# Kernel optimization log

Measured on AMD Instinct MI355X. Metric: run time of the kernel, lower is better.

Reference implementation:

```python
import jax, jax.numpy as jnp
import numpy as np

B, T, D = 32, 512, 1024
N = 65536
H, L = 150, 17


def setup_inputs() -> dict:
    key = jax.random.key(0)
    ks = jax.random.split(key, 5)
    xs = jax.random.normal(ks[0], (B, T, D), dtype=jnp.float32)
    spans = jax.random.randint(ks[1], (N, 2), 0, T, dtype=jnp.int64 if jax.config.jax_enable_x64 else jnp.int32)
    batch_ids = jax.random.randint(ks[2], (N,), 0, B, dtype=spans.dtype)
    W1 = jax.random.normal(ks[3], (2 * D, H), dtype=jnp.float32) / np.sqrt(2 * D)
    b1 = jnp.zeros((H,), dtype=jnp.float32)
    W2 = jax.random.normal(ks[4], (H, L), dtype=jnp.float32) / np.sqrt(H)
    b2 = jnp.zeros((L,), dtype=jnp.float32)
    return {"xs": xs, "spans": spans, "batch_ids": batch_ids,
            "W1": W1, "b1": b1, "W2": W2, "b2": b2}


def reference(xs, spans, batch_ids, W1, b1, W2, b2):
    # Flatten batch/time: xs_flat [B*T, D]; offset span indices into flat space,
    # mirroring `idxs + max_length * i` in the torch forward.
    d = xs.shape[-1]
    xs_flat = xs.reshape(-1, d)
    flat_idx = spans + batch_ids[:, None] * xs.shape[1]  # [N, 2]
    # feature == 'concat': gather begin/end token reps and concat -> [N, 2D]
    feats = xs_flat[flat_idx.reshape(-1)].reshape(flat_idx.shape[0], 2 * d)
    h = jax.nn.relu(feats @ W1 + b1)  # MLP hidden layer (dropout p=0)
    scores = h @ W2 + b2              # output layer, no activation
    return scores  # [N, num_labels]; torch.split is a zero-copy view, omitted
```

## Files before the change

### kernel.cpp

```cpp
#include <hip/hip_runtime.h>
#include <stdint.h>

#define TT 512
#define DD 1024
#define NN 65536
#define HH 150
#define LL 17

typedef __bf16 bf16_t;
typedef short shortx8 __attribute__((ext_vector_type(8)));
typedef short shortx4 __attribute__((ext_vector_type(4)));
typedef float f32x4 __attribute__((ext_vector_type(4)));

typedef __attribute__((address_space(1))) const void gconst_void;
typedef __attribute__((address_space(3))) void lds_void;

static __device__ __forceinline__ short f2bf(float f) {
  return (short)__builtin_bit_cast(unsigned short, (bf16_t)f);
}

__global__ __launch_bounds__(256) void prep_all(
    const float* __restrict__ xs, const float* __restrict__ W1,
    const float* __restrict__ W2, short* __restrict__ xs16,
    short* __restrict__ Bp, short* __restrict__ W2p, int do_cvt)
{
  int b = blockIdx.x;
  if (do_cvt && b < 2048) {
    int t = b * 256 + threadIdx.x;
#pragma unroll
    for (int i = 0; i < 8; ++i) {
      int id = t + i * 524288;
      f32x4 v = reinterpret_cast<const f32x4*>(xs)[id];
      shortx4 o;
      o[0] = f2bf(v[0]); o[1] = f2bf(v[1]); o[2] = f2bf(v[2]); o[3] = f2bf(v[3]);
      reinterpret_cast<shortx4*>(xs16)[id] = o;
    }
    return;
  }
  int rb = do_cvt ? b - 2048 : b;
  int task = rb * 256 + threadIdx.x;
  const int NW1 = 64 * 10 * 64;
  if (task < NW1) {
    int kb  = task / 640;
    int rem = task - kb * 640;
    int cb = rem >> 6, l = rem & 63;
    int col  = cb * 16 + (l & 15);
    int krow = kb * 32 + (l >> 4) * 8;
    shortx8 v;
#pragma unroll
    for (int j = 0; j < 8; ++j) {
      float f = (col < HH) ? W1[(krow + j) * HH + col] : 0.f;
      v[j] = f2bf(f);
    }
    *reinterpret_cast<shortx8*>(Bp + task * 8) = v;
  } else if (task < NW1 + 640) {
    int t2 = task - NW1;
    int kb  = t2 >> 7;
    int rem = t2 & 127;
    int cb = rem >> 6, l = rem & 63;
    int col  = cb * 16 + (l & 15);
    int krow = kb * 32 + (l >> 4) * 8;
    shortx8 v;
#pragma unroll
    for (int j = 0; j < 8; ++j) {
      int r = krow + j;
      float f = (r < HH && col < LL) ? W2[r * LL + col] : 0.f;
      v[j] = f2bf(f);
    }
    *reinterpret_cast<shortx8*>(W2p + t2 * 8) = v;
  }
}

__device__ __forceinline__ void stageB(const short* __restrict__ Bp, char* lds,
                                       int c, int p, int wv, int lane) {
#pragma unroll
  for (int i = 0; i < 5; ++i) {
    const char* g = (const char*)Bp + (size_t)c * 20480 + wv * 5120 + i * 1024 + lane * 16;
    char* l = lds + p * 20480 + wv * 5120 + i * 1024;
    __builtin_amdgcn_global_load_lds((gconst_void*)g, (lds_void*)l, 16, 0, 0);
  }
}

template<int XS16>
__device__ __forceinline__ void loadA(const char* const (&abase)[2][2], int c,
                                      int kg, shortx8 (&abuf)[2][2]) {
  const int side = (c >= 16) ? 1 : 0;
#pragma unroll
  for (int rf = 0; rf < 2; ++rf) {
#pragma unroll
    for (int s = 0; s < 2; ++s) {
      int ks31 = (2 * c + s) & 31;
      if constexpr (XS16) {
        abuf[rf][s] = *reinterpret_cast<const shortx8*>(
            abase[rf][side] + ks31 * 64 + kg * 16);
      } else {
        f32x4 x = *reinterpret_cast<const f32x4*>(abase[rf][side] + ks31 * 128 + kg * 32);
        f32x4 y = *reinterpret_cast<const f32x4*>(abase[rf][side] + ks31 * 128 + kg * 32 + 16);
        shortx8 t;
        t[0]=f2bf(x[0]); t[1]=f2bf(x[1]); t[2]=f2bf(x[2]); t[3]=f2bf(x[3]);
        t[4]=f2bf(y[0]); t[5]=f2bf(y[1]); t[6]=f2bf(y[2]); t[7]=f2bf(y[3]);
        abuf[rf][s] = t;
      }
    }
  }
}

__device__ __forceinline__ void computeC(const char* lds, int p, int lane,
                                         const shortx8 (&abuf)[2][2],
                                         f32x4 (&acc)[2][10]) {
#pragma unroll
  for (int s = 0; s < 2; ++s) {
    shortx8 bfr[10];
#pragma unroll
    for (int cb = 0; cb < 10; ++cb)
      bfr[cb] = *reinterpret_cast<const shortx8*>(
          lds + p * 20480 + (s * 10 + cb) * 1024 + lane * 16);
#pragma unroll
    for (int rf = 0; rf < 2; ++rf)
#pragma unroll
      for (int cb = 0; cb < 10; ++cb)
        acc[rf][cb] = __builtin_amdgcn_mfma_f32_16x16x32_bf16(
            abuf[rf][s], bfr[cb], acc[rf][cb], 0, 0, 0);
  }
}

template<int XS16>
__global__ __launch_bounds__(256, 1) void span_mlp2(
    const void* __restrict__ xsv, const int* __restrict__ spans,
    const int* __restrict__ bids, const short* __restrict__ Bp,
    const float* __restrict__ b1, const short* __restrict__ W2p,
    const float* __restrict__ b2, float* __restrict__ out)
{
  __shared__ __align__(16) char lds[43008];

  const int tid  = threadIdx.x;
  const int wv   = tid >> 6;
  const int lane = tid & 63;
  const int l15  = lane & 15;
  const int kg   = lane >> 4;
  const int blk  = blockIdx.x;

  const char* abase[2][2];
  const int elt = XS16 ? 2 : 4;
#pragma unroll
  for (int rf = 0; rf < 2; ++rf) {
    int r  = blk * 128 + wv * 32 + rf * 16 + l15;
    int bb = bids[r];
    int s0 = spans[2 * r + 0];
    int s1 = spans[2 * r + 1];
    abase[rf][0] = (const char*)xsv + (size_t)(bb * TT + s0) * DD * elt;
    abase[rf][1] = (const char*)xsv + (size_t)(bb * TT + s1) * DD * elt;
  }

  f32x4 acc[2][10];
  {
    f32x4 z = {0.f, 0.f, 0.f, 0.f};
#pragma unroll
    for (int rf = 0; rf < 2; ++rf)
#pragma unroll
      for (int cb = 0; cb < 10; ++cb) acc[rf][cb] = z;
  }

  shortx8 abufA[2][2], abufB[2][2];

#define WAITSTAGE() do { \
    if constexpr (XS16) asm volatile("s_waitcnt vmcnt(4)" ::: "memory"); \
    else                asm volatile("s_waitcnt vmcnt(8)" ::: "memory"); \
    __builtin_amdgcn_s_barrier(); \
    __builtin_amdgcn_sched_barrier(0); \
  } while (0)

  stageB(Bp, lds, 0, 0, wv, lane);
  loadA<XS16>(abase, 0, kg, abufA);
  WAITSTAGE();

  for (int cp = 0; cp < 16; ++cp) {
    int c0 = 2 * cp;
    stageB(Bp, lds, c0 + 1, 1, wv, lane);
    loadA<XS16>(abase, c0 + 1, kg, abufB);
    computeC(lds, 0, lane, abufA, acc);
    WAITSTAGE();
    if (cp < 15) {
      stageB(Bp, lds, c0 + 2, 0, wv, lane);
      loadA<XS16>(abase, c0 + 2, kg, abufA);
    }
    computeC(lds, 1, lane, abufB, acc);
    if (cp < 15) WAITSTAGE();
  }

  asm volatile("s_waitcnt vmcnt(0) lgkmcnt(0)" ::: "memory");
  __builtin_amdgcn_s_barrier();
  __builtin_amdgcn_sched_barrier(0);

  short* hW = reinterpret_cast<short*>(lds) + wv * 5376;
#pragma unroll
  for (int rf = 0; rf < 2; ++rf) {
#pragma unroll
    for (int cb = 0; cb < 10; ++cb) {
      int col = cb * 16 + l15;
      float bb = (col < HH) ? b1[col] : 0.f;
#pragma unroll
      for (int i = 0; i < 4; ++i) {
        int row = rf * 16 + kg * 4 + i;
        float v = fmaxf(acc[rf][cb][i] + bb, 0.f);
        hW[row * 168 + col] = f2bf(v);
      }
    }
  }

  f32x4 acc2[2][2];
  {
    f32x4 z = {0.f, 0.f, 0.f, 0.f};
#pragma unroll
    for (int rf = 0; rf < 2; ++rf) { acc2[rf][0] = z; acc2[rf][1] = z; }
  }
#pragma unroll
  for (int ks = 0; ks < 5; ++ks) {
#pragma unroll
    for (int cb2 = 0; cb2 < 2; ++cb2) {
      shortx8 wf = *reinterpret_cast<const shortx8*>(
          W2p + ((ks * 2 + cb2) * 64 + lane) * 8);
#pragma unroll
      for (int rf = 0; rf < 2; ++rf) {
        shortx8 af = *reinterpret_cast<const shortx8*>(
            reinterpret_cast<const char*>(hW) + (rf * 16 + l15) * 336 + ks * 64 + kg * 16);
        acc2[rf][cb2] = __builtin_amdgcn_mfma_f32_16x16x32_bf16(
            af, wf, acc2[rf][cb2], 0, 0, 0);
      }
    }
  }

#pragma unroll
  for (int rf = 0; rf < 2; ++rf) {
#pragma unroll
    for (int cb2 = 0; cb2 < 2; ++cb2) {
      int col = cb2 * 16 + l15;
      if (col < LL) {
        float bb = b2[col];
#pragma unroll
        for (int i = 0; i < 4; ++i) {
          int row = blk * 128 + wv * 32 + rf * 16 + kg * 4 + i;
          out[(size_t)row * LL + col] = acc2[rf][cb2][i] + bb;
        }
      }
    }
  }
#undef WAITSTAGE
}

extern "C" void kernel_launch(void* const* d_in, const int* in_sizes, int n_in,
                              void* d_out, int out_size, void* d_ws, size_t ws_size,
                              hipStream_t stream) {
  const float* xs    = (const float*)d_in[0];
  const int*   spans = (const int*)d_in[1];
  const int*   bids  = (const int*)d_in[2];
  const float* W1    = (const float*)d_in[3];
  const float* b1    = (const float*)d_in[4];
  const float* W2    = (const float*)d_in[5];
  const float* b2    = (const float*)d_in[6];
  float* out = (float*)d_out;

  const size_t XS16B = 33554432;
  const size_t WREQ  = XS16B + 655360 + 10240;

  if (ws_size >= WREQ) {
    short* xs16 = (short*)d_ws;
    short* Bp   = (short*)((char*)d_ws + XS16B);
    short* W2p  = Bp + 327680;
    prep_all<<<2211, 256, 0, stream>>>(xs, W1, W2, xs16, Bp, W2p, 1);
    span_mlp2<1><<<512, 256, 0, stream>>>(xs16, spans, bids, Bp, b1, W2p, b2, out);
  } else {
    short* Bp  = (short*)d_ws;
    short* W2p = Bp + 327680;
    prep_all<<<163, 256, 0, stream>>>(xs, W1, W2, nullptr, Bp, W2p, 0);
    span_mlp2<0><<<512, 256, 0, stream>>>(xs, spans, bids, Bp, b1, W2p, b2, out);
  }
}
```

Before: 159.4 us.

## Split waves 2x2 over rows/columns and load W1 fragments directly from global

Reorganizes the main GEMM so the four waves form a 2x2 grid: each wave computes 64 rows by 80 hidden columns, so every gathered feature fragment is reused across 5 column blocks and every W1 fragment across 4 row blocks. W1 fragments are now read straight from global/L2 into registers instead of being staged in LDS with async copies and per-step barriers, and the MFMA operand order is swapped so the result is stored transposed. The block also asks for 2 waves-per-SIMD occupancy, with only an occasional barrier to keep waves loosely in step. The trade-off is more global-load traffic for W1 (each wave fetches its half independently) and register pressure from the 20 accumulators plus double buffers under the tighter launch bound.

```diff
diff --git a/kernel.cpp b/kernel.cpp
--- a/kernel.cpp
+++ b/kernel.cpp
@@ -11,9 +11,6 @@
 typedef short shortx8 __attribute__((ext_vector_type(8)));
 typedef short shortx4 __attribute__((ext_vector_type(4)));
 typedef float f32x4 __attribute__((ext_vector_type(4)));
-
-typedef __attribute__((address_space(1))) const void gconst_void;
-typedef __attribute__((address_space(3))) void lds_void;
 
 static __device__ __forceinline__ short f2bf(float f) {
   return (short)__builtin_bit_cast(unsigned short, (bf16_t)f);
@@ -71,61 +68,8 @@
   }
 }
 
-__device__ __forceinline__ void stageB(const short* __restrict__ Bp, char* lds,
-                                       int c, int p, int wv, int lane) {
-#pragma unroll
-  for (int i = 0; i < 5; ++i) {
-    const char* g = (const char*)Bp + (size_t)c * 20480 + wv * 5120 + i * 1024 + lane * 16;
-    char* l = lds + p * 20480 + wv * 5120 + i * 1024;
-    __builtin_amdgcn_global_load_lds((gconst_void*)g, (lds_void*)l, 16, 0, 0);
-  }
-}
-
 template<int XS16>
-__device__ __forceinline__ void loadA(const char* const (&abase)[2][2], int c,
-                                      int kg, shortx8 (&abuf)[2][2]) {
-  const int side = (c >= 16) ? 1 : 0;
-#pragma unroll
-  for (int rf = 0; rf < 2; ++rf) {
-#pragma unroll
-    for (int s = 0; s < 2; ++s) {
-      int ks31 = (2 * c + s) & 31;
-      if constexpr (XS16) {
-        abuf[rf][s] = *reinterpret_cast<const shortx8*>(
-            abase[rf][side] + ks31 * 64 + kg * 16);
-      } else {
-        f32x4 x = *reinterpret_cast<const f32x4*>(abase[rf][side] + ks31 * 128 + kg * 32);
-        f32x4 y = *reinterpret_cast<const f32x4*>(abase[rf][side] + ks31 * 128 + kg * 32 + 16);
-        shortx8 t;
-        t[0]=f2bf(x[0]); t[1]=f2bf(x[1]); t[2]=f2bf(x[2]); t[3]=f2bf(x[3]);
-        t[4]=f2bf(y[0]); t[5]=f2bf(y[1]); t[6]=f2bf(y[2]); t[7]=f2bf(y[3]);
-        abuf[rf][s] = t;
-      }
-    }
-  }
-}
-
-__device__ __forceinline__ void computeC(const char* lds, int p, int lane,
-                                         const shortx8 (&abuf)[2][2],
-                                         f32x4 (&acc)[2][10]) {
-#pragma unroll
-  for (int s = 0; s < 2; ++s) {
-    shortx8 bfr[10];
-#pragma unroll
-    for (int cb = 0; cb < 10; ++cb)
-      bfr[cb] = *reinterpret_cast<const shortx8*>(
-          lds + p * 20480 + (s * 10 + cb) * 1024 + lane * 16);
-#pragma unroll
-    for (int rf = 0; rf < 2; ++rf)
-#pragma unroll
-      for (int cb = 0; cb < 10; ++cb)
-        acc[rf][cb] = __builtin_amdgcn_mfma_f32_16x16x32_bf16(
-            abuf[rf][s], bfr[cb], acc[rf][cb], 0, 0, 0);
-  }
-}
-
-template<int XS16>
-__global__ __launch_bounds__(256, 1) void span_mlp2(
+__global__ __launch_bounds__(256, 2) void span_mlp3(
     const void* __restrict__ xsv, const int* __restrict__ spans,
     const int* __restrict__ bids, const short* __restrict__ Bp,
     const float* __restrict__ b1, const short* __restrict__ W2p,
@@ -135,16 +79,18 @@
 
   const int tid  = threadIdx.x;
   const int wv   = tid >> 6;
+  const int wr   = wv >> 1;
+  const int wc   = wv & 1;
   const int lane = tid & 63;
   const int l15  = lane & 15;
   const int kg   = lane >> 4;
   const int blk  = blockIdx.x;
 
-  const char* abase[2][2];
+  const char* abase[4][2];
   const int elt = XS16 ? 2 : 4;
 #pragma unroll
-  for (int rf = 0; rf < 2; ++rf) {
-    int r  = blk * 128 + wv * 32 + rf * 16 + l15;
+  for (int rf = 0; rf < 4; ++rf) {
+    int r  = blk * 128 + wr * 64 + rf * 16 + l15;
     int bb = bids[r];
     int s0 = spans[2 * r + 0];
     int s1 = spans[2 * r + 1];
@@ -152,100 +98,116 @@
     abase[rf][1] = (const char*)xsv + (size_t)(bb * TT + s1) * DD * elt;
   }
 
-  f32x4 acc[2][10];
+  const char* bp = (const char*)Bp + (wc * 5) * 1024 + lane * 16;
+
+  f32x4 acc[4][5];
   {
     f32x4 z = {0.f, 0.f, 0.f, 0.f};
 #pragma unroll
-    for (int rf = 0; rf < 2; ++rf)
-#pragma unroll
-      for (int cb = 0; cb < 10; ++cb) acc[rf][cb] = z;
-  }
-
-  shortx8 abufA[2][2], abufB[2][2];
-
-#define WAITSTAGE() do { \
-    if constexpr (XS16) asm volatile("s_waitcnt vmcnt(4)" ::: "memory"); \
-    else                asm volatile("s_waitcnt vmcnt(8)" ::: "memory"); \
-    __builtin_amdgcn_s_barrier(); \
-    __builtin_amdgcn_sched_barrier(0); \
+    for (int rf = 0; rf < 4; ++rf)
+#pragma unroll
+      for (int cb = 0; cb < 5; ++cb) acc[rf][cb] = z;
+  }
+
+  shortx8 w1A[5], w1B[5], ftA[4], ftB[4];
+
+#define LOADW1(buf, g) do { _Pragma("unroll") \
+    for (int cb = 0; cb < 5; ++cb) \
+      buf[cb] = *reinterpret_cast<const shortx8*>(bp + ((g) * 10 + cb) * 1024); \
   } while (0)
 
-  stageB(Bp, lds, 0, 0, wv, lane);
-  loadA<XS16>(abase, 0, kg, abufA);
-  WAITSTAGE();
-
-  for (int cp = 0; cp < 16; ++cp) {
-    int c0 = 2 * cp;
-    stageB(Bp, lds, c0 + 1, 1, wv, lane);
-    loadA<XS16>(abase, c0 + 1, kg, abufB);
-    computeC(lds, 0, lane, abufA, acc);
-    WAITSTAGE();
-    if (cp < 15) {
-      stageB(Bp, lds, c0 + 2, 0, wv, lane);
-      loadA<XS16>(abase, c0 + 2, kg, abufA);
-    }
-    computeC(lds, 1, lane, abufB, acc);
-    if (cp < 15) WAITSTAGE();
-  }
-
-  asm volatile("s_waitcnt vmcnt(0) lgkmcnt(0)" ::: "memory");
-  __builtin_amdgcn_s_barrier();
-  __builtin_amdgcn_sched_barrier(0);
-
-  short* hW = reinterpret_cast<short*>(lds) + wv * 5376;
-#pragma unroll
-  for (int rf = 0; rf < 2; ++rf) {
-#pragma unroll
-    for (int cb = 0; cb < 10; ++cb) {
-      int col = cb * 16 + l15;
-      float bb = (col < HH) ? b1[col] : 0.f;
-#pragma unroll
-      for (int i = 0; i < 4; ++i) {
-        int row = rf * 16 + kg * 4 + i;
-        float v = fmaxf(acc[rf][cb][i] + bb, 0.f);
-        hW[row * 168 + col] = f2bf(v);
-      }
-    }
-  }
-
-  f32x4 acc2[2][2];
+#define LOADFT(buf, g) do { \
+    const int side_ = ((g) >= 32) ? 1 : 0; \
+    const int ko_ = ((g) & 31) * (XS16 ? 64 : 128) + kg * (XS16 ? 16 : 32); \
+    _Pragma("unroll") \
+    for (int rf = 0; rf < 4; ++rf) { \
+      if constexpr (XS16) { \
+        buf[rf] = *reinterpret_cast<const shortx8*>(abase[rf][side_] + ko_); \
+      } else { \
+        f32x4 x_ = *reinterpret_cast<const f32x4*>(abase[rf][side_] + ko_); \
+        f32x4 y_ = *reinterpret_cast<const f32x4*>(abase[rf][side_] + ko_ + 16); \
+        shortx8 t_; \
+        t_[0]=f2bf(x_[0]); t_[1]=f2bf(x_[1]); t_[2]=f2bf(x_[2]); t_[3]=f2bf(x_[3]); \
+        t_[4]=f2bf(y_[0]); t_[5]=f2bf(y_[1]); t_[6]=f2bf(y_[2]); t_[7]=f2bf(y_[3]); \
+        buf[rf] = t_; \
+      } \
+    } \
+  } while (0)
+
+#define MFMA_STEP(w1, ft) do { _Pragma("unroll") \
+    for (int rf = 0; rf < 4; ++rf) \
+      _Pragma("unroll") \
+      for (int cb = 0; cb < 5; ++cb) \
+        acc[rf][cb] = __builtin_amdgcn_mfma_f32_16x16x32_bf16( \
+            w1[cb], ft[rf], acc[rf][cb], 0, 0, 0); \
+  } while (0)
+
+  LOADW1(w1A, 0);
+  LOADFT(ftA, 0);
+  for (int gp = 0; gp < 32; ++gp) {
+    int g = 2 * gp;
+    LOADW1(w1B, g + 1);
+    LOADFT(ftB, g + 1);
+    MFMA_STEP(w1A, ftA);
+    if (gp < 31) {
+      LOADW1(w1A, g + 2);
+      LOADFT(ftA, g + 2);
+    }
+    MFMA_STEP(w1B, ftB);
+    if ((gp & 3) == 3) __builtin_amdgcn_s_barrier();
+  }
+#undef LOADW1
+#undef LOADFT
+#undef MFMA_STEP
+
+  short* hS = (short*)lds;
+#pragma unroll
+  for (int cb = 0; cb < 5; ++cb) {
+    f32x4 bv = *reinterpret_cast<const f32x4*>(b1 + wc * 80 + cb * 16 + kg * 4);
+#pragma unroll
+    for (int rf = 0; rf < 4; ++rf) {
+      f32x4 v = acc[rf][cb] + bv;
+      shortx4 hv;
+      hv[0] = f2bf(fmaxf(v[0], 0.f));
+      hv[1] = f2bf(fmaxf(v[1], 0.f));
+      hv[2] = f2bf(fmaxf(v[2], 0.f));
+      hv[3] = f2bf(fmaxf(v[3], 0.f));
+      int row = wr * 64 + rf * 16 + l15;
+      int col = wc * 80 + cb * 16 + kg * 4;
+      *reinterpret_cast<shortx4*>((char*)hS + row * 336 + col * 2) = hv;
+    }
+  }
+  __syncthreads();
+
+  f32x4 acc2[4];
   {
     f32x4 z = {0.f, 0.f, 0.f, 0.f};
 #pragma unroll
-    for (int rf = 0; rf < 2; ++rf) { acc2[rf][0] = z; acc2[rf][1] = z; }
+    for (int rf = 0; rf < 4; ++rf) acc2[rf] = z;
   }
 #pragma unroll
   for (int ks = 0; ks < 5; ++ks) {
-#pragma unroll
-    for (int cb2 = 0; cb2 < 2; ++cb2) {
-      shortx8 wf = *reinterpret_cast<const shortx8*>(
-          W2p + ((ks * 2 + cb2) * 64 + lane) * 8);
-#pragma unroll
-      for (int rf = 0; rf < 2; ++rf) {
-        shortx8 af = *reinterpret_cast<const shortx8*>(
-            reinterpret_cast<const char*>(hW) + (rf * 16 + l15) * 336 + ks * 64 + kg * 16);
-        acc2[rf][cb2] = __builtin_amdgcn_mfma_f32_16x16x32_bf16(
-            af, wf, acc2[rf][cb2], 0, 0, 0);
+    shortx8 wf = *reinterpret_cast<const shortx8*>(
+        W2p + ((ks * 2 + wc) * 64 + lane) * 8);
+#pragma unroll
+    for (int rf = 0; rf < 4; ++rf) {
+      shortx8 af = *reinterpret_cast<const shortx8*>(
+          (const char*)hS + (wr * 64 + rf * 16 + l15) * 336 + ks * 64 + kg * 16);
+      acc2[rf] = __builtin_amdgcn_mfma_f32_16x16x32_bf16(af, wf, acc2[rf], 0, 0, 0);
+    }
+  }
+
+  int col = wc * 16 + l15;
+  if (col < LL) {
+    float bb = b2[col];
+#pragma unroll
+    for (int rf = 0; rf < 4; ++rf)
+#pragma unroll
+      for (int i = 0; i < 4; ++i) {
+        int row = blk * 128 + wr * 64 + rf * 16 + kg * 4 + i;
+        out[(size_t)row * LL + col] = acc2[rf][i] + bb;
       }
-    }
-  }
-
-#pragma unroll
-  for (int rf = 0; rf < 2; ++rf) {
-#pragma unroll
-    for (int cb2 = 0; cb2 < 2; ++cb2) {
-      int col = cb2 * 16 + l15;
-      if (col < LL) {
-        float bb = b2[col];
-#pragma unroll
-        for (int i = 0; i < 4; ++i) {
-          int row = blk * 128 + wv * 32 + rf * 16 + kg * 4 + i;
-          out[(size_t)row * LL + col] = acc2[rf][cb2][i] + bb;
-        }
-      }
-    }
-  }
-#undef WAITSTAGE
+  }
 }
 
 extern "C" void kernel_launch(void* const* d_in, const int* in_sizes, int n_in,
@@ -268,11 +230,11 @@
     short* Bp   = (short*)((char*)d_ws + XS16B);
     short* W2p  = Bp + 327680;
     prep_all<<<2211, 256, 0, stream>>>(xs, W1, W2, xs16, Bp, W2p, 1);
-    span_mlp2<1><<<512, 256, 0, stream>>>(xs16, spans, bids, Bp, b1, W2p, b2, out);
+    span_mlp3<1><<<512, 256, 0, stream>>>(xs16, spans, bids, Bp, b1, W2p, b2, out);
   } else {
     short* Bp  = (short*)d_ws;
     short* W2p = Bp + 327680;
     prep_all<<<163, 256, 0, stream>>>(xs, W1, W2, nullptr, Bp, W2p, 0);
-    span_mlp2<0><<<512, 256, 0, stream>>>(xs, spans, bids, Bp, b1, W2p, b2, out);
-  }
-}
+    span_mlp3<0><<<512, 256, 0, stream>>>(xs, spans, bids, Bp, b1, W2p, b2, out);
+  }
+}
```

Measured after the change: 206.8 us. 29.7% more time.
